# Optimization experiments

Hardware: AMD Instinct MI355X
Metric: run time of the kernel (lower is better)

The kernel has to match this reference:

```python
import jax, jax.numpy as jnp
import numpy as np

N_NODES = 100000
N_EDGES = 1600000
D_IN = 32
D_OUT = 32
K_HOPS = 2
CUTGRAPH = 0.2
EPS = 1e-12  # torch F.normalize eps


def setup_inputs() -> dict:
    key = jax.random.key(0)
    k1, k2, k3, k4 = jax.random.split(key, 4)
    features = jax.random.normal(k1, (N_NODES, D_IN), dtype=jnp.float32)
    W = jax.random.normal(k2, (D_OUT, D_IN), dtype=jnp.float32) * (1.0 / np.sqrt(D_IN))
    src = jax.random.randint(k3, (N_EDGES,), 0, N_NODES, dtype=jnp.int64 if jax.config.jax_enable_x64 else jnp.int32)
    dst = jax.random.randint(k4, (N_EDGES,), 0, N_NODES, dtype=jnp.int64 if jax.config.jax_enable_x64 else jnp.int32)
    return {"features": features, "W": W, "src": src, "dst": dst}


def reference(features, W, src, dst):
    N = features.shape[0]
    E = src.shape[0]
    cut_k = int(E * CUTGRAPH)  # static edge count to prune

    # symmetric degree norm: deg^{-1/2} over in-degrees, clamped at 1
    deg = jax.ops.segment_sum(jnp.ones((E,), features.dtype), dst, num_segments=N)
    norm = jnp.power(jnp.clip(deg, 1.0, None), -0.5)[:, None]  # [N,1]

    h = features
    for _ in range(K_HOPS):
        # cosine-similarity edge pruning: zero the cut_k lowest-cos edges
        nrm = jnp.linalg.norm(h, axis=-1, keepdims=True)
        nh = h / jnp.maximum(nrm, EPS)  # F.normalize(p=2)
        cos = jnp.sum(nh[src] * nh[dst], axis=-1)  # [E]
        _, low_idx = jax.lax.top_k(-cos, cut_k)    # indices of smallest cos
        w = jnp.ones((E,), h.dtype).at[low_idx].set(0.0)

        h = h * norm
        msg = h[src] * w[:, None]                       # u_mul_e gather [E,D]
        h = jax.ops.segment_sum(msg, dst, num_segments=N)  # sum scatter
        h = h * norm

    return h @ W.T  # fc (bias=False)
```

## Files before the change

kernel.cpp:

```cpp
#include <hip/hip_runtime.h>
#include <hip/hip_bf16.h>
#include <stdint.h>

#define N_NODES 100000
#define N_EDGES 1600000
#define D_FEAT 32
#define CUT_K 320000
#define COSKEY_NB 3125
#define HC_NB 1000
#define HC_SLICE 1600
#define SCAN_NB ((N_NODES + 255) / 256)
#define TAILCAP 400000

#define PK(s, d, e) ((((unsigned long long)(s)) << 38) | \
                     (((unsigned long long)(d)) << 21) | (unsigned long long)(e))
#define PK_SRC(p) ((unsigned int)((p) >> 38))
#define PK_DST(p) ((unsigned int)(((p) >> 21) & 0x1FFFFu))
#define PK_EID(p) ((unsigned int)((p) & 0x1FFFFFu))

struct SelState { unsigned long long prefix; unsigned int k; };

__global__ void deg_kernel(const int* __restrict__ dst, int* __restrict__ deg,
                           int* __restrict__ rank, int E) {
    int e = blockIdx.x * blockDim.x + threadIdx.x;
    if (e < E) rank[e] = atomicAdd(&deg[dst[e]], 1);
}

__global__ void blocksum_kernel(const int* __restrict__ deg, int* __restrict__ bsum,
                                float* __restrict__ nrm, int N) {
    int i = blockIdx.x * 256 + threadIdx.x;
    int v = (i < N) ? deg[i] : 0;
    if (i < N) nrm[i] = 1.0f / sqrtf(fmaxf((float)v, 1.0f));
#pragma unroll
    for (int off = 32; off > 0; off >>= 1) v += __shfl_down(v, off, 64);
    __shared__ int ws4[4];
    if ((threadIdx.x & 63) == 0) ws4[threadIdx.x >> 6] = v;
    __syncthreads();
    if (threadIdx.x == 0) bsum[blockIdx.x] = ws4[0] + ws4[1] + ws4[2] + ws4[3];
}

__global__ void writeoffs_kernel(const int* __restrict__ deg, const int* __restrict__ bsum,
                                 int* __restrict__ offs, int N) {
    __shared__ int buf[256];
    __shared__ int ws4[4];
    __shared__ int sboff;
    int t = threadIdx.x;
    int b = blockIdx.x;
    int partial = 0;
    for (int i = t; i < b; i += 256) partial += bsum[i];
#pragma unroll
    for (int off = 32; off > 0; off >>= 1) partial += __shfl_down(partial, off, 64);
    if ((t & 63) == 0) ws4[t >> 6] = partial;
    __syncthreads();
    if (t == 0) sboff = ws4[0] + ws4[1] + ws4[2] + ws4[3];
    __syncthreads();
    int i = b * 256 + t;
    int v = (i < N) ? deg[i] : 0;
    buf[t] = v;
    __syncthreads();
    for (int off = 1; off < 256; off <<= 1) {
        int u = (t >= off) ? buf[t - off] : 0;
        __syncthreads();
        buf[t] += u;
        __syncthreads();
    }
    int ex = buf[t] - v + sboff;
    if (i < N) offs[i] = ex;
    if (i == N - 1) offs[N] = ex + v;
}

__global__ void fill_kernel(const int* __restrict__ src, const int* __restrict__ dst,
                            const int* __restrict__ rank, const int* __restrict__ offs,
                            unsigned long long* __restrict__ csr8, int E) {
    int e = blockIdx.x * blockDim.x + threadIdx.x;
    if (e >= E) return;
    int d = dst[e];
    int pos = offs[d] + rank[e];
    csr8[pos] = PK((unsigned int)src[e], (unsigned int)d, (unsigned int)e);
}

__global__ void rownorm_kernel(const float* __restrict__ h, float* __restrict__ nh, int N) {
    int i = blockIdx.x * blockDim.x + threadIdx.x;
    if (i >= N) return;
    const float4* hp = (const float4*)(h + (size_t)i * D_FEAT);
    float4 v[8];
    float ss = 0.f;
#pragma unroll
    for (int q = 0; q < 8; ++q) {
        v[q] = hp[q];
        ss += v[q].x * v[q].x + v[q].y * v[q].y + v[q].z * v[q].z + v[q].w * v[q].w;
    }
    float inv = 1.0f / fmaxf(sqrtf(ss), 1e-12f);
    float4* op = (float4*)(nh + (size_t)i * D_FEAT);
#pragma unroll
    for (int q = 0; q < 8; ++q) {
        float4 ov = v[q];
        ov.x *= inv; ov.y *= inv; ov.z *= inv; ov.w *= inv;
        op[q] = ov;
    }
}

__device__ __forceinline__ unsigned long long scan_select(
        const unsigned int* __restrict__ hist,
        unsigned long long pfx_in, unsigned int k_in,
        unsigned int* k_out) {
    __shared__ unsigned int sbuf[256];
    __shared__ unsigned long long s_pfx;
    __shared__ unsigned int s_k;
    int t = threadIdx.x;
    unsigned int s = hist[t];
    sbuf[t] = s;
    __syncthreads();
    for (int off = 1; off < 256; off <<= 1) {
        unsigned int v = (t >= off) ? sbuf[t - off] : 0u;
        __syncthreads();
        sbuf[t] += v;
        __syncthreads();
    }
    unsigned int incl = sbuf[t];
    unsigned int excl = incl - s;
    if (excl < k_in && k_in <= incl) {
        s_pfx = (pfx_in << 8) | (unsigned long long)t;
        s_k = k_in - excl;
    }
    __syncthreads();
    if (k_out) *k_out = s_k;
    return s_pfx;
}

__global__ void coskey_kernel(const float* __restrict__ nh,
                              const unsigned long long* __restrict__ csr8,
                              unsigned long long* __restrict__ keys,
                              unsigned int* __restrict__ hist0, int E) {
    __shared__ unsigned int lh[4][256];
    int t = threadIdx.x;
#pragma unroll
    for (int w = 0; w < 4; ++w) lh[w][t] = 0u;
    __syncthreads();
    int wave = t >> 6;
    int p0 = (blockIdx.x * 256 + t) * 2;
    unsigned long long r0 = csr8[p0];
    unsigned long long r1 = csr8[p0 + 1];
    const float4* a0 = (const float4*)(nh + (size_t)PK_SRC(r0) * D_FEAT);
    const float4* b0 = (const float4*)(nh + (size_t)PK_DST(r0) * D_FEAT);
    const float4* a1 = (const float4*)(nh + (size_t)PK_SRC(r1) * D_FEAT);
    const float4* b1 = (const float4*)(nh + (size_t)PK_DST(r1) * D_FEAT);
    float s0 = 0.f, s1 = 0.f;
#pragma unroll
    for (int q = 0; q < 8; ++q) {
        float4 x0 = a0[q], y0 = b0[q];
        s0 += x0.x * y0.x + x0.y * y0.y + x0.z * y0.z + x0.w * y0.w;
        float4 x1 = a1[q], y1 = b1[q];
        s1 += x1.x * y1.x + x1.y * y1.y + x1.z * y1.z + x1.w * y1.w;
    }
    unsigned int u0 = __float_as_uint(s0);
    unsigned int so0 = (u0 & 0x80000000u) ? ~u0 : (u0 | 0x80000000u);
    unsigned long long k0 = ((unsigned long long)so0 << 32) | PK_EID(r0);
    unsigned int u1 = __float_as_uint(s1);
    unsigned int so1 = (u1 & 0x80000000u) ? ~u1 : (u1 | 0x80000000u);
    unsigned long long k1 = ((unsigned long long)so1 << 32) | PK_EID(r1);
    *(ulonglong2*)(keys + p0) = make_ulonglong2(k0, k1);
    atomicAdd(&lh[wave][(unsigned int)(k0 >> 56)], 1u);
    atomicAdd(&lh[wave][(unsigned int)(k1 >> 56)], 1u);
    __syncthreads();
    unsigned int tot = lh[0][t] + lh[1][t] + lh[2][t] + lh[3][t];
    if (tot) atomicAdd(&hist0[t], tot);
}

__global__ void histc_kernel(const unsigned long long* __restrict__ in,
                             const int* __restrict__ cnt_in,
                             unsigned long long* __restrict__ out,
                             int* __restrict__ cnt_out,
                             const SelState* __restrict__ st_in,
                             SelState* __restrict__ st_out,
                             const unsigned int* __restrict__ hist_prev,
                             unsigned int* __restrict__ hist_cur, int pass) {
    __shared__ unsigned int lh[4][256];
    __shared__ unsigned int lcnt;
    int t = threadIdx.x, b = blockIdx.x;
#pragma unroll
    for (int w = 0; w < 4; ++w) lh[w][t] = 0u;
    if (t == 0) lcnt = 0u;

    unsigned long long pfx_in = st_in ? st_in->prefix : 0ull;
    unsigned int k_in = st_in ? st_in->k : (unsigned int)CUT_K;
    unsigned int k_cur;
    unsigned long long prefix = scan_select(hist_prev, pfx_in, k_in, &k_cur);
    if (b == 0 && t == 0) { st_out->prefix = prefix; st_out->k = k_cur; }
    __syncthreads();

    int n = cnt_in ? cnt_in[b] : HC_SLICE;
    const unsigned long long* sin = in + (size_t)b * HC_SLICE;
    unsigned long long* sout = out + (size_t)b * HC_SLICE;
    int wave = t >> 6;
    int fshift = 64 - 8 * pass;
    int dshift = 56 - 8 * pass;
    for (int i = t; i < n; i += 256) {
        unsigned long long key = sin[i];
        if ((key >> fshift) == prefix) {
            atomicAdd(&lh[wave][(unsigned int)((key >> dshift) & 0xFFull)], 1u);
            unsigned int slot = atomicAdd(&lcnt, 1u);
            sout[slot] = key;
        }
    }
    __syncthreads();
    if (t == 0) cnt_out[b] = (int)lcnt;
    unsigned int tot = lh[0][t] + lh[1][t] + lh[2][t] + lh[3][t];
    if (tot) atomicAdd(&hist_cur[t], tot);
}

__global__ void tail_kernel(const unsigned long long* __restrict__ in_sl,
                            const int* __restrict__ cnt_in,
                            unsigned long long* __restrict__ dense,
                            const SelState* __restrict__ st2,
                            const unsigned int* __restrict__ hist2,
                            unsigned long long* __restrict__ kth_out) {
    __shared__ unsigned int lh[256];
    __shared__ unsigned int sbuf[256];
    __shared__ unsigned long long s_pfx;
    __shared__ unsigned int s_k;
    __shared__ unsigned int s_n;
    int t = threadIdx.x;

    unsigned long long pfx = st2->prefix;
    unsigned int k = st2->k;
    {
        unsigned int s = hist2[t];
        sbuf[t] = s;
        __syncthreads();
        for (int off = 1; off < 256; off <<= 1) {
            unsigned int v = (t >= off) ? sbuf[t - off] : 0u;
            __syncthreads();
            sbuf[t] += v;
            __syncthreads();
        }
        unsigned int incl = sbuf[t], excl = incl - s;
        if (excl < k && k <= incl) { s_pfx = (pfx << 8) | (unsigned long long)t; s_k = k - excl; }
        __syncthreads();
        pfx = s_pfx; k = s_k;
        __syncthreads();
    }

    unsigned int n_in = 0;
    for (int pass = 3; pass < 8; ++pass) {
        lh[t] = 0u;
        if (t == 0) s_n = 0u;
        __syncthreads();
        int fshift = 64 - 8 * pass;
        int dshift = 56 - 8 * pass;
        unsigned long long* outp = dense + ((pass & 1) ? 0 : TAILCAP);
        if (pass == 3) {
            for (int b = t; b < HC_NB; b += 256) {
                int n = cnt_in[b];
                const unsigned long long* sl = in_sl + (size_t)b * HC_SLICE;
                for (int i = 0; i < n; ++i) {
                    unsigned long long key = sl[i];
                    if ((key >> fshift) == pfx) {
                        atomicAdd(&lh[(unsigned int)((key >> dshift) & 0xFFull)], 1u);
                        unsigned int slot = atomicAdd(&s_n, 1u);
                        if (slot < TAILCAP) outp[slot] = key;
                    }
                }
            }
        } else {
            const unsigned long long* inp = dense + ((pass & 1) ? TAILCAP : 0);
            for (unsigned int i = t; i < n_in; i += 256) {
                unsigned long long key = inp[i];
                if ((key >> fshift) == pfx) {
                    atomicAdd(&lh[(unsigned int)((key >> dshift) & 0xFFull)], 1u);
                    unsigned int slot = atomicAdd(&s_n, 1u);
                    if (slot < TAILCAP) outp[slot] = key;
                }
            }
        }
        __syncthreads();
        n_in = s_n;
        unsigned int s = lh[t];
        sbuf[t] = s;
        __syncthreads();
        for (int off = 1; off < 256; off <<= 1) {
            unsigned int v = (t >= off) ? sbuf[t - off] : 0u;
            __syncthreads();
            sbuf[t] += v;
            __syncthreads();
        }
        unsigned int incl = sbuf[t], excl = incl - s;
        if (excl < k && k <= incl) { s_pfx = (pfx << 8) | (unsigned long long)t; s_k = k - excl; }
        __syncthreads();
        pfx = s_pfx; k = s_k;
        __syncthreads();
    }
    if (t == 0) *kth_out = pfx;
}

template<bool FUSE_FC>
__global__ void aggregate_csr_kernel(const float* __restrict__ h_in, float* __restrict__ h_out,
                                     const int* __restrict__ offs,
                                     const unsigned long long* __restrict__ csr8,
                                     const unsigned long long* __restrict__ keys,
                                     const unsigned long long* __restrict__ kth_in,
                                     const float* __restrict__ nrm,
                                     const float* __restrict__ W, int N) {
    __shared__ float Ws[32][33];
    __shared__ float hrow[8][33];
    int t = threadIdx.x;
    if (FUSE_FC) {
        for (int i = t; i < 1024; i += 256) Ws[i >> 5][i & 31] = W[i];
        __syncthreads();
    }
    unsigned long long kth = *kth_in;
    int g = blockIdx.x * 8 + (t >> 5);
    int j = t & 31;
    if (!FUSE_FC && g >= N) return;
    int lo = offs[g], hi = offs[g + 1];
    float acc = 0.f;
    int p = lo;
    for (; p + 8 <= hi; p += 8) {
        unsigned long long kk[8];
        unsigned int ss[8];
#pragma unroll
        for (int u = 0; u < 8; ++u) { kk[u] = keys[p + u]; ss[u] = PK_SRC(csr8[p + u]); }
        float vv[8];
#pragma unroll
        for (int u = 0; u < 8; ++u) vv[u] = h_in[(size_t)ss[u] * D_FEAT + j] * nrm[ss[u]];
#pragma unroll
        for (int u = 0; u < 8; ++u) acc += (kk[u] > kth) ? vv[u] : 0.f;
    }
    for (; p < hi; ++p) {
        if (keys[p] > kth) {
            unsigned int s = PK_SRC(csr8[p]);
            acc += h_in[(size_t)s * D_FEAT + j] * nrm[s];
        }
    }
    float val = acc * nrm[g];
    if (!FUSE_FC) {
        h_out[(size_t)g * D_FEAT + j] = val;
        return;
    }
    hrow[t >> 5][j] = val;
    __syncthreads();
    float oacc = 0.f;
#pragma unroll
    for (int q = 0; q < 32; ++q) oacc += hrow[t >> 5][q] * Ws[j][q];
    h_out[(size_t)g * D_FEAT + j] = oacc;
}

extern "C" void kernel_launch(void* const* d_in, const int* in_sizes, int n_in,
                              void* d_out, int out_size, void* d_ws, size_t ws_size,
                              hipStream_t stream) {
    const float* features = (const float*)d_in[0];
    const float* W        = (const float*)d_in[1];
    const int*   src      = (const int*)d_in[2];
    const int*   dst      = (const int*)d_in[3];
    float*       out      = (float*)d_out;

    char* ws = (char*)d_ws;
    size_t o = 0;
    auto take = [&](size_t bytes) -> char* {
        char* p = ws + o;
        o += (bytes + 255) & ~(size_t)255;
        return p;
    };
    int*                deg     = (int*)take((size_t)N_NODES * 4);
    float*              nrm     = (float*)take((size_t)N_NODES * 4);
    int*                offs    = (int*)take((size_t)(N_NODES + 1) * 4);
    int*                rank    = (int*)take((size_t)N_EDGES * 4);
    unsigned long long* csr8    = (unsigned long long*)take((size_t)N_EDGES * 8);
    float*              hA      = (float*)take((size_t)N_NODES * D_FEAT * 4);
    float*              nh      = (float*)take((size_t)N_NODES * D_FEAT * 4);
    unsigned long long* keys    = (unsigned long long*)take((size_t)N_EDGES * 8);
    unsigned long long* candA   = (unsigned long long*)take((size_t)HC_NB * HC_SLICE * 8);
    unsigned long long* candB   = (unsigned long long*)take((size_t)HC_NB * HC_SLICE * 8);
    unsigned int*       hist    = (unsigned int*)take((size_t)16 * 256 * 4);
    SelState*           stArr   = (SelState*)take((size_t)16 * sizeof(SelState));
    unsigned long long* kthbuf  = (unsigned long long*)take(256);
    int*                bsum    = (int*)take((size_t)SCAN_NB * 4);
    int*                cnt_a   = (int*)take((size_t)HC_NB * 4);
    int*                cnt_b   = (int*)take((size_t)HC_NB * 4);

    hipMemsetAsync(deg, 0, (size_t)N_NODES * 4, stream);
    hipMemsetAsync(hist, 0, (size_t)16 * 256 * 4, stream);

    deg_kernel<<<(N_EDGES + 255) / 256, 256, 0, stream>>>(dst, deg, rank, N_EDGES);
    blocksum_kernel<<<SCAN_NB, 256, 0, stream>>>(deg, bsum, nrm, N_NODES);
    writeoffs_kernel<<<SCAN_NB, 256, 0, stream>>>(deg, bsum, offs, N_NODES);
    fill_kernel<<<(N_EDGES + 255) / 256, 256, 0, stream>>>(src, dst, rank, offs, csr8, N_EDGES);

    const float* hin = features;
    for (int hop = 0; hop < 2; ++hop) {
        unsigned int* hh = hist + (size_t)hop * 8 * 256;
        SelState*     hst = stArr + (size_t)hop * 8;
        rownorm_kernel<<<(N_NODES + 255) / 256, 256, 0, stream>>>(hin, nh, N_NODES);
        coskey_kernel<<<COSKEY_NB, 256, 0, stream>>>(nh, csr8, keys, hh, N_EDGES);
        histc_kernel<<<HC_NB, 256, 0, stream>>>(keys, nullptr, candA, cnt_a,
                                                nullptr, hst + 1,
                                                hh + 0 * 256, hh + 1 * 256, 1);
        histc_kernel<<<HC_NB, 256, 0, stream>>>(candA, cnt_a, candB, cnt_b,
                                                hst + 1, hst + 2,
                                                hh + 1 * 256, hh + 2 * 256, 2);
        tail_kernel<<<1, 256, 0, stream>>>(candB, cnt_b, candA,
                                           hst + 2, hh + 2 * 256, kthbuf + hop);
        if (hop == 0) {
            aggregate_csr_kernel<false><<<(N_NODES + 7) / 8, 256, 0, stream>>>(
                hin, hA, offs, csr8, keys, kthbuf + hop, nrm, nullptr, N_NODES);
            hin = hA;
        } else {
            aggregate_csr_kernel<true><<<(N_NODES + 7) / 8, 256, 0, stream>>>(
                hin, out, offs, csr8, keys, kthbuf + hop, nrm, W, N_NODES);
        }
    }
}
```

Measured before the change: 509.1 us.

## Fuse CSR fill with first rownorm, double histogram blocks, unroll aggregate by 16

Merges the CSR fill kernel with the hop-0 row normalisation into one launch split by block index, removing one kernel launch and letting the two independent jobs overlap. Doubles the number of histogram/compaction blocks and halves each slice, giving more parallelism in the selection passes. Adds a 16-wide unrolled gather loop in the aggregation kernel to put more loads in flight, at the cost of higher register pressure.

```diff
diff --git a/kernel.cpp b/kernel.cpp
--- a/kernel.cpp
+++ b/kernel.cpp
@@ -7,8 +7,9 @@
 #define D_FEAT 32
 #define CUT_K 320000
 #define COSKEY_NB 3125
-#define HC_NB 1000
-#define HC_SLICE 1600
+#define FILL_NB 6250
+#define HC_NB 2000
+#define HC_SLICE 800
 #define SCAN_NB ((N_NODES + 255) / 256)
 #define TAILCAP 400000
 
@@ -69,19 +70,8 @@
     if (i == N - 1) offs[N] = ex + v;
 }
 
-__global__ void fill_kernel(const int* __restrict__ src, const int* __restrict__ dst,
-                            const int* __restrict__ rank, const int* __restrict__ offs,
-                            unsigned long long* __restrict__ csr8, int E) {
-    int e = blockIdx.x * blockDim.x + threadIdx.x;
-    if (e >= E) return;
-    int d = dst[e];
-    int pos = offs[d] + rank[e];
-    csr8[pos] = PK((unsigned int)src[e], (unsigned int)d, (unsigned int)e);
-}
-
-__global__ void rownorm_kernel(const float* __restrict__ h, float* __restrict__ nh, int N) {
-    int i = blockIdx.x * blockDim.x + threadIdx.x;
-    if (i >= N) return;
+__device__ __forceinline__ void rownorm_row(const float* __restrict__ h,
+                                            float* __restrict__ nh, int i) {
     const float4* hp = (const float4*)(h + (size_t)i * D_FEAT);
     float4 v[8];
     float ss = 0.f;
@@ -98,6 +88,28 @@
         ov.x *= inv; ov.y *= inv; ov.z *= inv; ov.w *= inv;
         op[q] = ov;
     }
+}
+
+__global__ void fill_rownorm_kernel(const int* __restrict__ src, const int* __restrict__ dst,
+                                    const int* __restrict__ rank, const int* __restrict__ offs,
+                                    unsigned long long* __restrict__ csr8,
+                                    const float* __restrict__ h, float* __restrict__ nh,
+                                    int E, int N) {
+    int b = blockIdx.x;
+    if (b < FILL_NB) {
+        int e = b * 256 + threadIdx.x;
+        int d = dst[e];
+        int pos = offs[d] + rank[e];
+        csr8[pos] = PK((unsigned int)src[e], (unsigned int)d, (unsigned int)e);
+    } else {
+        int i = (b - FILL_NB) * 256 + threadIdx.x;
+        if (i < N) rownorm_row(h, nh, i);
+    }
+}
+
+__global__ void rownorm_kernel(const float* __restrict__ h, float* __restrict__ nh, int N) {
+    int i = blockIdx.x * blockDim.x + threadIdx.x;
+    if (i < N) rownorm_row(h, nh, i);
 }
 
 __device__ __forceinline__ unsigned long long scan_select(
@@ -315,6 +327,17 @@
     int lo = offs[g], hi = offs[g + 1];
     float acc = 0.f;
     int p = lo;
+    for (; p + 16 <= hi; p += 16) {
+        unsigned long long kk[16];
+        unsigned int ss[16];
+#pragma unroll
+        for (int u = 0; u < 16; ++u) { kk[u] = keys[p + u]; ss[u] = PK_SRC(csr8[p + u]); }
+        float vv[16];
+#pragma unroll
+        for (int u = 0; u < 16; ++u) vv[u] = h_in[(size_t)ss[u] * D_FEAT + j] * nrm[ss[u]];
+#pragma unroll
+        for (int u = 0; u < 16; ++u) acc += (kk[u] > kth) ? vv[u] : 0.f;
+    }
     for (; p + 8 <= hi; p += 8) {
         unsigned long long kk[8];
         unsigned int ss[8];
@@ -384,13 +407,15 @@
     deg_kernel<<<(N_EDGES + 255) / 256, 256, 0, stream>>>(dst, deg, rank, N_EDGES);
     blocksum_kernel<<<SCAN_NB, 256, 0, stream>>>(deg, bsum, nrm, N_NODES);
     writeoffs_kernel<<<SCAN_NB, 256, 0, stream>>>(deg, bsum, offs, N_NODES);
-    fill_kernel<<<(N_EDGES + 255) / 256, 256, 0, stream>>>(src, dst, rank, offs, csr8, N_EDGES);
+    fill_rownorm_kernel<<<FILL_NB + SCAN_NB, 256, 0, stream>>>(
+        src, dst, rank, offs, csr8, features, nh, N_EDGES, N_NODES);
 
     const float* hin = features;
     for (int hop = 0; hop < 2; ++hop) {
         unsigned int* hh = hist + (size_t)hop * 8 * 256;
         SelState*     hst = stArr + (size_t)hop * 8;
-        rownorm_kernel<<<(N_NODES + 255) / 256, 256, 0, stream>>>(hin, nh, N_NODES);
+        if (hop == 1)
+            rownorm_kernel<<<SCAN_NB, 256, 0, stream>>>(hin, nh, N_NODES);
         coskey_kernel<<<COSKEY_NB, 256, 0, stream>>>(nh, csr8, keys, hh, N_EDGES);
         histc_kernel<<<HC_NB, 256, 0, stream>>>(keys, nullptr, candA, cnt_a,
                                                 nullptr, hst + 1,
```

Result: slower. 615.4 us (+20.9%).
